# Performance work log

Hardware: AMD Instinct MI355X
Metric: run time of the kernel (lower is better)

## Reference

```python
import jax, jax.numpy as jnp
import numpy as np

B, N, SIG_DIM, K = 128, 200000, 192, 32


def _l2norm(x):
    return x / jnp.linalg.norm(x, axis=-1, keepdims=True)


def setup_inputs() -> dict:
    key = jax.random.key(0)
    kq, kg, km = jax.random.split(key, 3)
    # queries and gallery signatures are L2-normalised per the docstring
    query_signature = _l2norm(jax.random.normal(kq, (B, SIG_DIM), dtype=jnp.float32))
    gallery_sigs = _l2norm(jax.random.normal(kg, (N, SIG_DIM), dtype=jnp.float32))
    exclude_mask = jax.random.bernoulli(km, p=0.01, shape=(B, N))
    return {
        "query_signature": query_signature,
        "gallery_sigs": gallery_sigs,
        "exclude_mask": exclude_mask,
        "k": K,
    }


def reference(query_signature, gallery_sigs, exclude_mask, k):
    # Equivalent to the chunked running top-k merge in Gallery.retrieve:
    # cosine-sim scores (inputs pre-normalised), masked fill -inf, global top-k.
    scores = query_signature @ gallery_sigs.T              # [B, N]
    scores = jnp.where(exclude_mask, -jnp.inf, scores)
    top_scores, top_idx = jax.lax.top_k(scores, k)          # [B, k] each
    return top_idx.astype(jnp.int64), top_scores
```

## Files before the change

kernel.cpp:

```cpp
#include <hip/hip_runtime.h>
#include <hip/hip_bf16.h>
#include <cstdint>
#include <cstddef>

#define BQ 128
#define DK 192
#define KTOP 32
#define CHI 64
#define QCAP 512
#define CAP 8192
#define OCAP 65536
#define MARGIN 0.02f
#define SCN 768
#define THRV 3200

#define NEG_INF (-__builtin_huge_valf())

typedef short short8v __attribute__((ext_vector_type(8)));
typedef float f32x16  __attribute__((ext_vector_type(16)));

__device__ __forceinline__ unsigned fkey(float s) {
    unsigned u = __float_as_uint(s);
    return (u & 0x80000000u) ? ~u : (u | 0x80000000u);
}
__device__ __forceinline__ bool pri_gt(float s1, int i1, float s2, int i2) {
    return (s1 > s2) || (s1 == s2 && i1 < i2);
}
__device__ __forceinline__ unsigned pk_trunc(float a, float b) {
    return __builtin_amdgcn_perm(__float_as_uint(b), __float_as_uint(a),
                                 0x07060302u);
}
__device__ __forceinline__ unsigned f2bf_rne(float x) {
    unsigned u = __float_as_uint(x);
    unsigned r = u + 0x7FFFu + ((u >> 16) & 1u);
    return r >> 16;
}
__device__ __forceinline__ float dot192(const float* __restrict__ a,
                                        const float* __restrict__ b) {
    float s = 0.f;
    #pragma unroll 8
    for (int k = 0; k < DK; ++k) s = fmaf(a[k], b[k], s);
    return s;
}
__device__ __forceinline__ void gload_lds16(const void* g, void* l) {
    __builtin_amdgcn_global_load_lds(
        (const __attribute__((address_space(1))) unsigned int*)g,
        (__attribute__((address_space(3))) unsigned int*)l,
        16, 0, 0);
}

__global__ __launch_bounds__(256) void qprep(
    const float* __restrict__ Qf, unsigned short* __restrict__ Qi)
{
    const int b = blockIdx.x * 256 + threadIdx.x;
    if (b >= 12 * 256) return;
    const int s = b >> 8, w = (b >> 6) & 3, lane = b & 63;
    const int q  = w * 32 + (lane & 31);
    const int k0 = (lane >> 5) * 8 + s * 16;
    const float* qp = Qf + q * DK + k0;
    unsigned short* dst = Qi + (size_t)b * 8;
    #pragma unroll
    for (int e = 0; e < 8; ++e) dst[e] = (unsigned short)f2bf_rne(qp[e]);
}

template<int MODE>
__global__ __launch_bounds__(256, 2) void score_pass(
    const float* __restrict__ Qf, const unsigned short* __restrict__ Qi,
    const float* __restrict__ G,
    const int* __restrict__ mask, const float* __restrict__ thrm,
    float* __restrict__ gmax,
    int* __restrict__ gcnt, float* __restrict__ cs, int* __restrict__ ci,
    int* __restrict__ ocnt, int* __restrict__ oq, int* __restrict__ og,
    float* __restrict__ osv,
    int Ntot, int NCH, int SC)
{
    __shared__ float    Gf[CHI * DK];
    __shared__ float    thrmS[BQ];
    __shared__ unsigned queue[QCAP];
    __shared__ int      qn;

    const int t = threadIdx.x;
    const int w = t >> 6, lane = t & 63;
    const int lo5 = lane & 31, hi = lane >> 5;
    const int qbW = w * 32;

    const int chunk = (MODE == 0)
        ? (int)(((long long)blockIdx.x * NCH) / SC)
        : (int)blockIdx.x;
    const int cb = chunk * CHI;

    #pragma unroll
    for (int i = 0; i < 12; ++i) {
        const int slot = t + (i << 8);
        const int r = slot / 48, c = slot - r * 48;
        size_t grow = (size_t)cb + r;
        if (grow >= (size_t)Ntot) grow = (size_t)Ntot - 1;
        const char* gp = (const char*)G + grow * (DK * 4) + ((c ^ (r & 7)) << 4);
        char* lp = (char*)Gf + ((i << 2) + w) * 1024;
        gload_lds16(gp, lp);
    }

    uint4 aF[12];
    {
        const uint4* qp = reinterpret_cast<const uint4*>(Qi) + (w << 6) + lane;
        #pragma unroll
        for (int s = 0; s < 12; ++s)
            aF[s] = qp[s << 8];
    }
    #pragma unroll
    for (int s = 0; s < 12; ++s)
        asm volatile("" : "+v"(aF[s].x), "+v"(aF[s].y),
                          "+v"(aF[s].z), "+v"(aF[s].w));

    if (t < BQ) thrmS[t] = (MODE == 1) ? thrm[t] : 0.f;
    if (t == 0) qn = 0;
    __syncthreads();

    const unsigned xsh = (unsigned)((lo5 & 7) << 4);
    const char* rowp0 = (const char*)Gf + lo5 * (DK * 4);
    const char* rowp1 = (const char*)Gf + (32 + lo5) * (DK * 4);

    f32x16 acc[2] = {
        {0,0,0,0,0,0,0,0,0,0,0,0,0,0,0,0}, {0,0,0,0,0,0,0,0,0,0,0,0,0,0,0,0}};
    #pragma unroll
    for (int s = 0; s < 12; ++s) {
        const unsigned b0 = ((unsigned)((s * 4 + hi * 2) << 4)) ^ xsh;
        const unsigned b1 = ((unsigned)((s * 4 + hi * 2 + 1) << 4)) ^ xsh;
        union { uint4 u; short8v v; } au; au.u = aF[s];
        {
            float4 f0 = *reinterpret_cast<const float4*>(rowp0 + b0);
            float4 f1 = *reinterpret_cast<const float4*>(rowp0 + b1);
            union { unsigned u[4]; short8v v; } bu;
            bu.u[0] = pk_trunc(f0.x, f0.y); bu.u[1] = pk_trunc(f0.z, f0.w);
            bu.u[2] = pk_trunc(f1.x, f1.y); bu.u[3] = pk_trunc(f1.z, f1.w);
            acc[0] = __builtin_amdgcn_mfma_f32_32x32x16_bf16(au.v, bu.v, acc[0], 0, 0, 0);
        }
        {
            float4 f0 = *reinterpret_cast<const float4*>(rowp1 + b0);
            float4 f1 = *reinterpret_cast<const float4*>(rowp1 + b1);
            union { unsigned u[4]; short8v v; } bu;
            bu.u[0] = pk_trunc(f0.x, f0.y); bu.u[1] = pk_trunc(f0.z, f0.w);
            bu.u[2] = pk_trunc(f1.x, f1.y); bu.u[3] = pk_trunc(f1.z, f1.w);
            acc[1] = __builtin_amdgcn_mfma_f32_32x32x16_bf16(au.v, bu.v, acc[1], 0, 0, 0);
        }
    }

    if (MODE == 0) {
        #pragma unroll
        for (int j = 0; j < 16; ++j) {
            const int row = (j & 3) + 8 * (j >> 2) + 4 * hi;
            const int q = qbW + row;
            const size_t mrow = (size_t)q * (size_t)Ntot;
            float m = NEG_INF;
            #pragma unroll
            for (int st = 0; st < 2; ++st) {
                const int g = cb + st * 32 + lo5;
                if (g < Ntot && !mask[mrow + g]) m = fmaxf(m, acc[st][j]);
            }
            #pragma unroll
            for (int off = 1; off < 32; off <<= 1)
                m = fmaxf(m, __shfl_xor(m, off));
            if (lo5 == 0) gmax[(size_t)blockIdx.x * BQ + q] = m;
        }
    } else {
        #pragma unroll
        for (int j = 0; j < 16; ++j) {
            const int row = (j & 3) + 8 * (j >> 2) + 4 * hi;
            const int q = qbW + row;
            const float th = thrmS[q];
            #pragma unroll
            for (int st = 0; st < 2; ++st) {
                const int g = cb + st * 32 + lo5;
                const float s = acc[st][j];
                if (g < Ntot && s >= th) {
                    if (!mask[(size_t)q * (size_t)Ntot + g]) {
                        const int p = atomicAdd(&qn, 1);
                        if (p < QCAP) {
                            queue[p] = ((unsigned)q << 24) | (unsigned)g;
                        } else {
                            float sx = dot192(Qf + q * DK, G + (size_t)g * DK);
                            const int op = atomicAdd(ocnt, 1);
                            if (op < OCAP) { oq[op] = q; og[op] = g; osv[op] = sx; }
                        }
                    }
                }
            }
        }
        __syncthreads();
        const int nq = qn < QCAP ? qn : QCAP;
        for (int cc = w; cc < nq; cc += 4) {
            const unsigned pk = queue[cc];
            const int q = pk >> 24, gg = pk & 0xFFFFFF;
            const float* qr = Qf + q * DK;
            const float* gr = G + (size_t)gg * DK;
            const int k0 = lane * 3;
            float part = qr[k0] * gr[k0];
            part = fmaf(qr[k0 + 1], gr[k0 + 1], part);
            part = fmaf(qr[k0 + 2], gr[k0 + 2], part);
            #pragma unroll
            for (int off = 32; off > 0; off >>= 1)
                part += __shfl_xor(part, off);
            if (lane == 0) {
                const int pos = atomicAdd(&gcnt[q * 16], 1);
                if (pos < CAP) {
                    cs[(size_t)q * CAP + pos] = part;
                    ci[(size_t)q * CAP + pos] = gg;
                } else {
                    const int op = atomicAdd(ocnt, 1);
                    if (op < OCAP) { oq[op] = q; og[op] = gg; osv[op] = part; }
                }
            }
        }
    }
}

__global__ __launch_bounds__(256) void thr32(
    const float* __restrict__ gmax, float* __restrict__ thrm, int SC)
{
    __shared__ float vals[THRV];
    __shared__ int hist[256];
    __shared__ int hscan[256];
    __shared__ int bS, gtS;

    const int q = blockIdx.x;
    const int t = threadIdx.x;
    const int M = SC < THRV ? SC : THRV;

    for (int i = t; i < M; i += 256) {
        float m = gmax[(size_t)i * BQ + q];
        for (int j = i + THRV; j < SC; j += THRV)
            m = fmaxf(m, gmax[(size_t)j * BQ + q]);
        vals[i] = m;
    }
    __syncthreads();

    unsigned prefix = 0, pmask = 0;
    int kneed = KTOP;
    for (int pass = 0; pass < 4; ++pass) {
        const int shift = 24 - pass * 8;
        hist[t] = 0;
        __syncthreads();
        for (int i = t; i < M; i += 256) {
            unsigned k = fkey(vals[i]);
            if ((k & pmask) == prefix) atomicAdd(&hist[(k >> shift) & 255], 1);
        }
        __syncthreads();
        int* src = hist; int* dst = hscan;
        for (int off = 1; off < 256; off <<= 1) {
            int v = src[t] + ((t + off) < 256 ? src[t + off] : 0);
            __syncthreads();
            dst[t] = v;
            __syncthreads();
            int* tmp = src; src = dst; dst = tmp;
        }
        if (src[t] >= kneed && (t == 255 || src[t + 1] < kneed)) {
            bS = t; gtS = (t == 255) ? 0 : src[t + 1];
        }
        __syncthreads();
        kneed -= gtS;
        prefix |= ((unsigned)bS) << shift;
        pmask  |= 0xFFu << shift;
        __syncthreads();
    }
    if (t == 0) {
        unsigned u = (prefix & 0x80000000u) ? (prefix & 0x7FFFFFFFu) : ~prefix;
        thrm[q] = __uint_as_float(u) - MARGIN;
    }
}

__global__ __launch_bounds__(256) void select_topk(
    const float* __restrict__ cs, const int* __restrict__ ci,
    const int* __restrict__ gcnt,
    const int* __restrict__ ocnt, const int* __restrict__ oq,
    const int* __restrict__ og, const float* __restrict__ osv,
    float* __restrict__ out)
{
    __shared__ int   hist[256];
    __shared__ int   hscan[256];
    __shared__ float Ls[256];
    __shared__ int   Li[256];
    __shared__ int   lcnt, nTotS, bS, gtS;
    __shared__ float wrs[4]; __shared__ int wri[4], wrslot[4];

    const int q = blockIdx.x;
    const int t = threadIdx.x;
    const int n0 = gcnt[q * 16];
    const int n = n0 < CAP ? n0 : CAP;
    const size_t base = (size_t)q * CAP;
    const int novf0 = *ocnt;
    const int novf = novf0 < OCAP ? novf0 : OCAP;

    if (t == 0) nTotS = 0;
    __syncthreads();
    {
        int part = (t == 0) ? n : 0;
        for (int i = t; i < novf; i += 256)
            if (oq[i] == q) part++;
        atomicAdd(&nTotS, part);
    }
    __syncthreads();
    const int nTot = nTotS;

    unsigned prefix = 0, pmask = 0;
    int kneed = KTOP;

    if (nTot > KTOP) {
        for (int pass = 0; pass < 4; ++pass) {
            const int shift = 24 - pass * 8;
            hist[t] = 0;
            __syncthreads();
            for (int i = t; i < n; i += 256) {
                unsigned k = fkey(cs[base + i]);
                if ((k & pmask) == prefix)
                    atomicAdd(&hist[(k >> shift) & 255], 1);
            }
            for (int i = t; i < novf; i += 256) {
                if (oq[i] == q) {
                    unsigned k = fkey(osv[i]);
                    if ((k & pmask) == prefix)
                        atomicAdd(&hist[(k >> shift) & 255], 1);
                }
            }
            __syncthreads();
            int* src = hist; int* dst = hscan;
            for (int off = 1; off < 256; off <<= 1) {
                int v = src[t] + ((t + off) < 256 ? src[t + off] : 0);
                __syncthreads();
                dst[t] = v;
                __syncthreads();
                int* tmp = src; src = dst; dst = tmp;
            }
            if (src[t] >= kneed && (t == 255 || src[t + 1] < kneed)) {
                bS = t;
                gtS = (t == 255) ? 0 : src[t + 1];
            }
            __syncthreads();
            const int b = bS;
            kneed -= gtS;
            prefix |= ((unsigned)b) << shift;
            pmask  |= 0xFFu << shift;
            __syncthreads();
        }
    }

    if (t == 0) lcnt = 0;
    __syncthreads();
    const unsigned T = (nTot > KTOP) ? prefix : 0u;
    for (int i = t; i < n; i += 256) {
        float s = cs[base + i];
        if (fkey(s) >= T) {
            int p = atomicAdd(&lcnt, 1);
            if (p < 256) { Ls[p] = s; Li[p] = ci[base + i]; }
        }
    }
    for (int i = t; i < novf; i += 256) {
        if (oq[i] == q) {
            float s = osv[i];
            if (fkey(s) >= T) {
                int p = atomicAdd(&lcnt, 1);
                if (p < 256) { Ls[p] = s; Li[p] = og[i]; }
            }
        }
    }
    __syncthreads();
    const int M = lcnt < 256 ? lcnt : 256;

    const int w = t >> 6, lane = t & 63;
    for (int r = 0; r < KTOP; ++r) {
        float bv = (t < M) ? Ls[t] : NEG_INF;
        int   bi = (t < M) ? Li[t] : 0x7fffffff;
        int   bslot = t;
        #pragma unroll
        for (int off = 32; off > 0; off >>= 1) {
            float ov = __shfl_xor(bv, off);
            int   oi = __shfl_xor(bi, off);
            int   osl = __shfl_xor(bslot, off);
            if (pri_gt(ov, oi, bv, bi)) { bv = ov; bi = oi; bslot = osl; }
        }
        if (lane == 0) { wrs[w] = bv; wri[w] = bi; wrslot[w] = bslot; }
        __syncthreads();
        if (t == 0) {
            float fv = wrs[0]; int fi = wri[0]; int fs = wrslot[0];
            #pragma unroll
            for (int ww = 1; ww < 4; ++ww)
                if (pri_gt(wrs[ww], wri[ww], fv, fi)) {
                    fv = wrs[ww]; fi = wri[ww]; fs = wrslot[ww];
                }
            out[q * KTOP + r]                     = (float)fi;
            out[(size_t)BQ * KTOP + q * KTOP + r] = fv;
            Ls[fs] = NEG_INF; Li[fs] = 0x7fffffff;
        }
        __syncthreads();
    }
}

extern "C" void kernel_launch(void* const* d_in, const int* in_sizes, int n_in,
                              void* d_out, int out_size, void* d_ws, size_t ws_size,
                              hipStream_t stream)
{
    const float* Qf   = (const float*)d_in[0];
    const float* G    = (const float*)d_in[1];
    const int*   mask = (const int*)d_in[2];
    const int Ntot = in_sizes[1] / DK;

    const int NCH = (Ntot + CHI - 1) / CHI;
    int SC = SCN;
    if (SC > NCH) SC = NCH;

    char* w = (char*)d_ws;
    int*   ocnt = (int*)(w + 0);
    int*   gcnt = (int*)(w + 1024);
    float* thrm = (float*)(w + 10240);
    unsigned short* Qi = (unsigned short*)(w + 16384);
    size_t off = 16384 + (size_t)BQ * DK * 2;
    off = (off + 255) & ~(size_t)255;
    float* gmax = (float*)(w + off);
    off += (size_t)SC * BQ * 4; off = (off + 255) & ~(size_t)255;
    float* cs   = (float*)(w + off);
    off += (size_t)BQ * CAP * 4;
    int*   ci   = (int*)(w + off);
    off += (size_t)BQ * CAP * 4;
    int*   oqv  = (int*)(w + off);   off += (size_t)OCAP * 4;
    int*   ogv  = (int*)(w + off);   off += (size_t)OCAP * 4;
    float* osv  = (float*)(w + off);

    (void)hipMemsetAsync(w, 0, 16384, stream);
    qprep<<<dim3((12 * 256 + 255) / 256), dim3(256), 0, stream>>>(Qf, Qi);
    score_pass<0><<<dim3(SC), dim3(256), 0, stream>>>(
        Qf, Qi, G, mask, thrm, gmax, gcnt, cs, ci, ocnt, oqv, ogv, osv,
        Ntot, NCH, SC);
    thr32<<<dim3(BQ), dim3(256), 0, stream>>>(gmax, thrm, SC);
    score_pass<1><<<dim3(NCH), dim3(256), 0, stream>>>(
        Qf, Qi, G, mask, thrm, gmax, gcnt, cs, ci, ocnt, oqv, ogv, osv,
        Ntot, NCH, SC);
    select_topk<<<dim3(BQ), dim3(256), 0, stream>>>(
        cs, ci, gcnt, ocnt, oqv, ogv, osv, (float*)d_out);
}
```

Baseline: 130.5 us.

## Stage gallery chunk as bf16 in LDS via registers with smaller chunk

Replaces the direct global-to-LDS fp32 copy with register loads that convert to bf16 before storing into a swizzled LDS tile. This halves LDS footprint and LDS read traffic, and removes the per-MFMA fp32-to-bf16 packing in the inner loop. The gallery chunk per block also drops from 64 to 32 rows, so each block runs one accumulator tile instead of two. The cost is twice as many blocks with proportionally more per-block overhead (query fragment loads, threshold setup, reductions), plus the loss of the asynchronous direct-to-LDS load path.

```diff
diff --git a/kernel.cpp b/kernel.cpp
--- a/kernel.cpp
+++ b/kernel.cpp
@@ -6,7 +6,7 @@
 #define BQ 128
 #define DK 192
 #define KTOP 32
-#define CHI 64
+#define CHI 32
 #define QCAP 512
 #define CAP 8192
 #define OCAP 65536
@@ -41,12 +41,6 @@
     #pragma unroll 8
     for (int k = 0; k < DK; ++k) s = fmaf(a[k], b[k], s);
     return s;
-}
-__device__ __forceinline__ void gload_lds16(const void* g, void* l) {
-    __builtin_amdgcn_global_load_lds(
-        (const __attribute__((address_space(1))) unsigned int*)g,
-        (__attribute__((address_space(3))) unsigned int*)l,
-        16, 0, 0);
 }
 
 __global__ __launch_bounds__(256) void qprep(
@@ -74,7 +68,7 @@
     float* __restrict__ osv,
     int Ntot, int NCH, int SC)
 {
-    __shared__ float    Gf[CHI * DK];
+    __shared__ unsigned char Gb[CHI * 384];
     __shared__ float    thrmS[BQ];
     __shared__ unsigned queue[QCAP];
     __shared__ int      qn;
@@ -89,17 +83,19 @@
         : (int)blockIdx.x;
     const int cb = chunk * CHI;
 
-    #pragma unroll
-    for (int i = 0; i < 12; ++i) {
-        const int slot = t + (i << 8);
-        const int r = slot / 48, c = slot - r * 48;
-        size_t grow = (size_t)cb + r;
-        if (grow >= (size_t)Ntot) grow = (size_t)Ntot - 1;
-        const char* gp = (const char*)G + grow * (DK * 4) + ((c ^ (r & 7)) << 4);
-        char* lp = (char*)Gf + ((i << 2) + w) * 1024;
-        gload_lds16(gp, lp);
-    }
-
+    float4 ld[6];
+    int srow[6], sc4[6];
+    {
+        const float4* src = reinterpret_cast<const float4*>(G) + (size_t)cb * 48;
+        #pragma unroll
+        for (int i = 0; i < 6; ++i) {
+            const int slot = t + (i << 8);
+            const int r = slot / 48, c = slot - r * 48;
+            srow[i] = r; sc4[i] = c;
+            const int gr = (cb + r < Ntot) ? slot : (slot - (cb + r - (Ntot - 1)) * 48);
+            ld[i] = src[gr];
+        }
+    }
     uint4 aF[12];
     {
         const uint4* qp = reinterpret_cast<const uint4*>(Qi) + (w << 6) + lane;
@@ -112,51 +108,41 @@
         asm volatile("" : "+v"(aF[s].x), "+v"(aF[s].y),
                           "+v"(aF[s].z), "+v"(aF[s].w));
 
+    #pragma unroll
+    for (int i = 0; i < 6; ++i) {
+        const int r = srow[i], c = sc4[i];
+        const uint2 p = make_uint2(pk_trunc(ld[i].x, ld[i].y),
+                                   pk_trunc(ld[i].z, ld[i].w));
+        const int blk = (c >> 1) ^ (r & 7);
+        *reinterpret_cast<uint2*>(Gb + r * 384 + blk * 16 + (c & 1) * 8) = p;
+    }
+
     if (t < BQ) thrmS[t] = (MODE == 1) ? thrm[t] : 0.f;
     if (t == 0) qn = 0;
     __syncthreads();
 
     const unsigned xsh = (unsigned)((lo5 & 7) << 4);
-    const char* rowp0 = (const char*)Gf + lo5 * (DK * 4);
-    const char* rowp1 = (const char*)Gf + (32 + lo5) * (DK * 4);
-
-    f32x16 acc[2] = {
-        {0,0,0,0,0,0,0,0,0,0,0,0,0,0,0,0}, {0,0,0,0,0,0,0,0,0,0,0,0,0,0,0,0}};
+    const unsigned char* rowp = Gb + lo5 * 384;
+
+    f32x16 acc = {0,0,0,0,0,0,0,0,0,0,0,0,0,0,0,0};
     #pragma unroll
     for (int s = 0; s < 12; ++s) {
-        const unsigned b0 = ((unsigned)((s * 4 + hi * 2) << 4)) ^ xsh;
-        const unsigned b1 = ((unsigned)((s * 4 + hi * 2 + 1) << 4)) ^ xsh;
         union { uint4 u; short8v v; } au; au.u = aF[s];
-        {
-            float4 f0 = *reinterpret_cast<const float4*>(rowp0 + b0);
-            float4 f1 = *reinterpret_cast<const float4*>(rowp0 + b1);
-            union { unsigned u[4]; short8v v; } bu;
-            bu.u[0] = pk_trunc(f0.x, f0.y); bu.u[1] = pk_trunc(f0.z, f0.w);
-            bu.u[2] = pk_trunc(f1.x, f1.y); bu.u[3] = pk_trunc(f1.z, f1.w);
-            acc[0] = __builtin_amdgcn_mfma_f32_32x32x16_bf16(au.v, bu.v, acc[0], 0, 0, 0);
-        }
-        {
-            float4 f0 = *reinterpret_cast<const float4*>(rowp1 + b0);
-            float4 f1 = *reinterpret_cast<const float4*>(rowp1 + b1);
-            union { unsigned u[4]; short8v v; } bu;
-            bu.u[0] = pk_trunc(f0.x, f0.y); bu.u[1] = pk_trunc(f0.z, f0.w);
-            bu.u[2] = pk_trunc(f1.x, f1.y); bu.u[3] = pk_trunc(f1.z, f1.w);
-            acc[1] = __builtin_amdgcn_mfma_f32_32x32x16_bf16(au.v, bu.v, acc[1], 0, 0, 0);
-        }
-    }
-
+        union { uint4 u; short8v v; } bu;
+        bu.u = *reinterpret_cast<const uint4*>(
+            rowp + (((unsigned)((s * 2 + hi) << 4)) ^ xsh));
+        acc = __builtin_amdgcn_mfma_f32_32x32x16_bf16(au.v, bu.v, acc, 0, 0, 0);
+    }
+
+    const int g = cb + lo5;
     if (MODE == 0) {
         #pragma unroll
         for (int j = 0; j < 16; ++j) {
             const int row = (j & 3) + 8 * (j >> 2) + 4 * hi;
             const int q = qbW + row;
-            const size_t mrow = (size_t)q * (size_t)Ntot;
             float m = NEG_INF;
-            #pragma unroll
-            for (int st = 0; st < 2; ++st) {
-                const int g = cb + st * 32 + lo5;
-                if (g < Ntot && !mask[mrow + g]) m = fmaxf(m, acc[st][j]);
-            }
+            if (g < Ntot && !mask[(size_t)q * (size_t)Ntot + g])
+                m = acc[j];
             #pragma unroll
             for (int off = 1; off < 32; off <<= 1)
                 m = fmaxf(m, __shfl_xor(m, off));
@@ -168,20 +154,16 @@
             const int row = (j & 3) + 8 * (j >> 2) + 4 * hi;
             const int q = qbW + row;
             const float th = thrmS[q];
-            #pragma unroll
-            for (int st = 0; st < 2; ++st) {
-                const int g = cb + st * 32 + lo5;
-                const float s = acc[st][j];
-                if (g < Ntot && s >= th) {
-                    if (!mask[(size_t)q * (size_t)Ntot + g]) {
-                        const int p = atomicAdd(&qn, 1);
-                        if (p < QCAP) {
-                            queue[p] = ((unsigned)q << 24) | (unsigned)g;
-                        } else {
-                            float sx = dot192(Qf + q * DK, G + (size_t)g * DK);
-                            const int op = atomicAdd(ocnt, 1);
-                            if (op < OCAP) { oq[op] = q; og[op] = g; osv[op] = sx; }
-                        }
+            const float s = acc[j];
+            if (g < Ntot && s >= th) {
+                if (!mask[(size_t)q * (size_t)Ntot + g]) {
+                    const int p = atomicAdd(&qn, 1);
+                    if (p < QCAP) {
+                        queue[p] = ((unsigned)q << 24) | (unsigned)g;
+                    } else {
+                        float sx = dot192(Qf + q * DK, G + (size_t)g * DK);
+                        const int op = atomicAdd(ocnt, 1);
+                        if (op < OCAP) { oq[op] = q; og[op] = g; osv[op] = sx; }
                     }
                 }
             }
```

After: 123.7 us. 1.05x faster.
